# Performance work log

Measured on AMD Instinct MI355X. Metric: run time of the kernel, lower is better.

The kernel has to match this reference:

```python
import jax, jax.numpy as jnp
import numpy as np

B = 32768
IN_DIM = 768
HIDDENS = [2048, 1024, 512]
EMBED_DIM = 128
NUM_EMB = 1024
DEPTH = 3


def setup_inputs() -> dict:
    key = jax.random.key(0)
    ks = jax.random.split(key, 20)
    d = {"x": jax.random.normal(ks[0], (B, IN_DIM), dtype=jnp.float32)}
    # Encoder: in -> h0 -> h1 -> h2 -> embed  (weights stored as [in, out])
    enc_dims = [IN_DIM] + HIDDENS + [EMBED_DIM]
    for i in range(4):
        fan_in = enc_dims[i]
        d[f"enc_W{i+1}"] = jax.random.normal(ks[1 + i], (enc_dims[i], enc_dims[i + 1]), dtype=jnp.float32) / np.sqrt(fan_in)
        d[f"enc_b{i+1}"] = jnp.zeros((enc_dims[i + 1],), dtype=jnp.float32)
    # Decoder: embed -> h0 -> h1 -> h2 -> in
    dec_dims = [EMBED_DIM] + HIDDENS + [IN_DIM]
    for i in range(4):
        fan_in = dec_dims[i]
        d[f"dec_W{i+1}"] = jax.random.normal(ks[5 + i], (dec_dims[i], dec_dims[i + 1]), dtype=jnp.float32) / np.sqrt(fan_in)
        d[f"dec_b{i+1}"] = jnp.zeros((dec_dims[i + 1],), dtype=jnp.float32)
    # Codebook (nn.Embedding weight, initialized ~ N(0,1) as in the module)
    d["codebook"] = jax.random.normal(ks[9], (NUM_EMB, EMBED_DIM), dtype=jnp.float32)
    return d


def _encoder(x, W1, b1, W2, b2, W3, b3, W4, b4):
    x = jax.nn.relu(x @ W1 + b1)
    x = jax.nn.relu(x @ W2 + b2)
    x = jax.nn.relu(x @ W3 + b3)
    return x @ W4 + b4


def _decoder(x, W1, b1, W2, b2, W3, b3, W4, b4):
    x = jax.nn.relu(x @ W1 + b1)
    x = jax.nn.relu(x @ W2 + b2)
    x = jax.nn.relu(x @ W3 + b3)
    return x @ W4 + b4


def reference(x,
              enc_W1, enc_b1, enc_W2, enc_b2, enc_W3, enc_b3, enc_W4, enc_b4,
              dec_W1, dec_b1, dec_W2, dec_b2, dec_W3, dec_b3, dec_W4, dec_b4,
              codebook):
    z = _encoder(x, enc_W1, enc_b1, enc_W2, enc_b2, enc_W3, enc_b3, enc_W4, enc_b4)
    z_det = jax.lax.stop_gradient(z)

    cb_sq = jnp.sum(codebook * codebook, axis=1)  # [K]
    residue = z_det
    z_hat = jnp.zeros_like(z_det)
    codes = []
    for _ in range(DEPTH):  # residual quantization loop
        # squared L2 distances [B, K]
        dist = (jnp.sum(residue * residue, axis=1, keepdims=True)
                + cb_sq
                - 2.0 * residue @ codebook.T)
        idx = jnp.argmin(dist, axis=1)          # [B]
        codes.append(idx)
        z_hat = z_hat + codebook[idx]           # gather codebook vectors
        residue = z_det - z_hat
    all_codes = jnp.stack(codes, axis=1)        # [B, DEPTH] int

    # straight-through estimator: forward uses z_hat, grad flows through z
    z_flow = z + jax.lax.stop_gradient(z_hat - z)
    x_recon = _decoder(z_flow, dec_W1, dec_b1, dec_W2, dec_b2, dec_W3, dec_b3, dec_W4, dec_b4)
    return (x_recon, all_codes)
```

## Files before the change

kernel.cpp:

```cpp
#include <hip/hip_runtime.h>

#define FLT_MAX_C 3.402823466e+38f

typedef __attribute__((ext_vector_type(8))) __bf16 bf16x8;
typedef __attribute__((ext_vector_type(4))) float f32x4;

static __device__ __forceinline__ ushort f2bf(float x) {
    union { float f; unsigned u; } v; v.f = x;
    unsigned r = (v.u + 0x7FFFu + ((v.u >> 16) & 1u)) >> 16;
    return (ushort)r;
}

template<bool RELU, int TAG>
__global__ __launch_bounds__(256) void gemm_f32(
    const float* __restrict__ A, const float* __restrict__ W,
    const float* __restrict__ bias, float* __restrict__ C,
    int M, int K, int N)
{
    __shared__ float As[8][128];
    __shared__ float Bs[8][132];
    const int tid = threadIdx.x;
    const int bm = blockIdx.y << 7;
    const int bn = blockIdx.x << 7;

    const int la_row = tid >> 1;
    const int la_k   = (tid & 1) << 2;
    const int lb_row = tid >> 5;
    const int lb_col = (tid & 31) << 2;
    const int tm4 = (tid >> 4) << 2;
    const int tn4 = (tid & 15) << 2;

    float acc[8][8];
    #pragma unroll
    for (int i = 0; i < 8; ++i)
        #pragma unroll
        for (int j = 0; j < 8; ++j) acc[i][j] = 0.f;

    const float* aptr = A + (size_t)(bm + la_row) * K + la_k;
    const float* bptr = W + (size_t)lb_row * N + bn + lb_col;

    float4 av = *(const float4*)(aptr);
    float4 bv = *(const float4*)(bptr);

    for (int k0 = 0; k0 < K; k0 += 8) {
        __syncthreads();
        As[la_k + 0][la_row] = av.x;
        As[la_k + 1][la_row] = av.y;
        As[la_k + 2][la_row] = av.z;
        As[la_k + 3][la_row] = av.w;
        *(float4*)(&Bs[lb_row][lb_col]) = bv;
        __syncthreads();
        if (k0 + 8 < K) {
            av = *(const float4*)(aptr + k0 + 8);
            bv = *(const float4*)(bptr + (size_t)(k0 + 8) * N);
        }
        #pragma unroll
        for (int kk = 0; kk < 8; ++kk) {
            float a[8], b[8];
            *(float4*)(a)     = *(const float4*)(&As[kk][tm4]);
            *(float4*)(a + 4) = *(const float4*)(&As[kk][tm4 + 64]);
            *(float4*)(b)     = *(const float4*)(&Bs[kk][tn4]);
            *(float4*)(b + 4) = *(const float4*)(&Bs[kk][tn4 + 64]);
            #pragma unroll
            for (int i = 0; i < 8; ++i)
                #pragma unroll
                for (int j = 0; j < 8; ++j)
                    acc[i][j] = fmaf(a[i], b[j], acc[i][j]);
        }
    }

    float bv0[8];
    #pragma unroll
    for (int j = 0; j < 8; ++j)
        bv0[j] = bias[bn + tn4 + (j < 4 ? j : 60 + j)];

    #pragma unroll
    for (int i = 0; i < 8; ++i) {
        int row = bm + tm4 + (i < 4 ? i : 60 + i);
        float* cp = C + (size_t)row * N + bn + tn4;
        float4 v0, v1;
        v0.x = acc[i][0] + bv0[0]; v0.y = acc[i][1] + bv0[1];
        v0.z = acc[i][2] + bv0[2]; v0.w = acc[i][3] + bv0[3];
        v1.x = acc[i][4] + bv0[4]; v1.y = acc[i][5] + bv0[5];
        v1.z = acc[i][6] + bv0[6]; v1.w = acc[i][7] + bv0[7];
        if (RELU) {
            v0.x = fmaxf(v0.x, 0.f); v0.y = fmaxf(v0.y, 0.f);
            v0.z = fmaxf(v0.z, 0.f); v0.w = fmaxf(v0.w, 0.f);
            v1.x = fmaxf(v1.x, 0.f); v1.y = fmaxf(v1.y, 0.f);
            v1.z = fmaxf(v1.z, 0.f); v1.w = fmaxf(v1.w, 0.f);
        }
        *(float4*)(cp) = v0;
        *(float4*)(cp + 64) = v1;
    }
}

template<bool RELU, bool OUTF32, int TAG>
__global__ __launch_bounds__(256) void gemm_bf16(
    const ushort* __restrict__ A,
    const ushort* __restrict__ Wt,
    const float* __restrict__ bias,
    void* __restrict__ C,
    int M, int K, int N)
{
    __shared__ __align__(16) ushort As[128][64];
    __shared__ __align__(16) ushort Bs[128][64];
    const int tid  = threadIdx.x;
    const int lane = tid & 63;
    const int wv   = tid >> 6;
    const int wm   = (wv >> 1) << 6;
    const int wn   = (wv & 1) << 6;
    const int bm   = blockIdx.y << 7;
    const int bn   = blockIdx.x << 7;
    const int lr   = lane & 15;
    const int lh   = lane >> 4;

    f32x4 acc[4][4];
    #pragma unroll
    for (int m = 0; m < 4; ++m)
        #pragma unroll
        for (int n = 0; n < 4; ++n) acc[m][n] = (f32x4){0.f, 0.f, 0.f, 0.f};

    for (int k0 = 0; k0 < K; k0 += 64) {
        __syncthreads();
        #pragma unroll
        for (int i = 0; i < 4; ++i) {
            const int c    = wv * 4 + i;
            const int boff = c * 1024 + lane * 16;
            const int r    = boff >> 7;
            const int cbt  = boff & 127;
            const char* sa = (const char*)A  + (((size_t)(bm + r) * K + k0) << 1) + cbt;
            const char* sb = (const char*)Wt + (((size_t)(bn + r) * K + k0) << 1) + cbt;
            __builtin_amdgcn_global_load_lds((const void*)sa, (void*)(&As[0][0] + c * 512), 16, 0, 0);
            __builtin_amdgcn_global_load_lds((const void*)sb, (void*)(&Bs[0][0] + c * 512), 16, 0, 0);
        }
        __syncthreads();
        #pragma unroll
        for (int kk = 0; kk < 64; kk += 32) {
            bf16x8 af[4], bfr[4];
            #pragma unroll
            for (int m = 0; m < 4; ++m)
                af[m] = *(const bf16x8*)&As[wm + m * 16 + lr][kk + lh * 8];
            #pragma unroll
            for (int n = 0; n < 4; ++n)
                bfr[n] = *(const bf16x8*)&Bs[wn + n * 16 + lr][kk + lh * 8];
            #pragma unroll
            for (int m = 0; m < 4; ++m)
                #pragma unroll
                for (int n = 0; n < 4; ++n)
                    acc[m][n] = __builtin_amdgcn_mfma_f32_16x16x32_bf16(
                        af[m], bfr[n], acc[m][n], 0, 0, 0);
        }
    }

    #pragma unroll
    for (int n = 0; n < 4; ++n) {
        const int col = bn + wn + n * 16 + lr;
        const float bcol = bias[col];
        #pragma unroll
        for (int m = 0; m < 4; ++m) {
            #pragma unroll
            for (int i = 0; i < 4; ++i) {
                const int row = bm + wm + m * 16 + lh * 4 + i;
                float v = acc[m][n][i] + bcol;
                if (RELU) v = fmaxf(v, 0.f);
                if (OUTF32) ((float*)C)[(size_t)row * N + col] = v;
                else        ((ushort*)C)[(size_t)row * N + col] = f2bf(v);
            }
        }
    }
}

__global__ __launch_bounds__(256) void wt_convert(
    const float* __restrict__ W, ushort* __restrict__ Wt, int K, int N)
{
    __shared__ ushort t[64][65];
    const int kb = blockIdx.y << 6, nb = blockIdx.x << 6;
    const int c  = threadIdx.x & 63;
    const int r0 = (threadIdx.x >> 6) << 4;
    #pragma unroll
    for (int i = 0; i < 16; ++i)
        t[r0 + i][c] = f2bf(W[(size_t)(kb + r0 + i) * N + nb + c]);
    __syncthreads();
    #pragma unroll
    for (int i = 0; i < 16; ++i)
        Wt[(size_t)(nb + r0 + i) * K + kb + c] = t[c][r0 + i];
}

__global__ __launch_bounds__(256) void cbsq_kernel(
    const float* __restrict__ cb, float* __restrict__ cbsq)
{
    int k = blockIdx.x * 256 + threadIdx.x;
    const float* r = cb + ((size_t)k << 7);
    float s = 0.f;
    #pragma unroll 8
    for (int d = 0; d < 128; ++d) s = fmaf(r[d], r[d], s);
    cbsq[k] = s;
}

__global__ __launch_bounds__(256, 2) void quant_kernel(
    const float* __restrict__ z, const float* __restrict__ cb,
    const float* __restrict__ cbsq, ushort* __restrict__ zhat_bf,
    float* __restrict__ codes)
{
    __shared__ __align__(16) float cbl[2][4][16 * 128];
    __shared__ float sd[4][64];
    __shared__ int   si[4][64];

    const int lane = threadIdx.x & 63;
    const int wv   = threadIdx.x >> 6;
    const size_t row = (size_t)blockIdx.x * 64 + lane;
    const int kbeg = wv << 8;

    const float4* zr = (const float4*)(z + row * 128);
    float4 r[32];
    #pragma unroll
    for (int i = 0; i < 32; ++i) r[i] = zr[i];

    float mycb[4];
    #pragma unroll
    for (int j = 0; j < 4; ++j) mycb[j] = cbsq[kbeg + (j << 6) + lane];

    auto stage = [&](int c, int b) {
        const float* src = cb + ((size_t)(kbeg + (c << 4)) << 7);
        float* dst = &cbl[b][wv][0];
        #pragma unroll
        for (int i = 0; i < 8; ++i) {
            __builtin_amdgcn_global_load_lds(
                (const void*)(src + i * 256 + lane * 4),
                (void*)(dst + i * 256), 16, 0, 0);
        }
    };

    for (int t = 0; t < 3; ++t) {
        float4 rr4 = {0.f, 0.f, 0.f, 0.f};
        #pragma unroll
        for (int i = 0; i < 32; ++i) {
            rr4.x = fmaf(r[i].x, r[i].x, rr4.x);
            rr4.y = fmaf(r[i].y, r[i].y, rr4.y);
            rr4.z = fmaf(r[i].z, r[i].z, rr4.z);
            rr4.w = fmaf(r[i].w, r[i].w, rr4.w);
        }
        const float rr = (rr4.x + rr4.y) + (rr4.z + rr4.w);

        stage(0, 0);
        float bd = FLT_MAX_C; int bi = 0;
        for (int c = 0; c < 16; ++c) {
            if (c < 15) {
                stage(c + 1, (c + 1) & 1);
                asm volatile("s_waitcnt vmcnt(8)" ::: "memory");
            } else {
                asm volatile("s_waitcnt vmcnt(0)" ::: "memory");
            }
            const float* buf = cbl[c & 1][wv];
            for (int tt = 0; tt < 16; ++tt) {
                const float4* c4 = (const float4*)(buf + tt * 128);
                float4 a4 = {0.f, 0.f, 0.f, 0.f};
                #pragma unroll
                for (int i = 0; i < 32; ++i) {
                    float4 cv = c4[i];
                    a4.x = fmaf(r[i].x, cv.x, a4.x);
                    a4.y = fmaf(r[i].y, cv.y, a4.y);
                    a4.z = fmaf(r[i].z, cv.z, a4.z);
                    a4.w = fmaf(r[i].w, cv.w, a4.w);
                }
                float dot = (a4.x + a4.y) + (a4.z + a4.w);
                const int q = (c << 4) + tt;
                float cs = __shfl(mycb[q >> 6], q & 63);
                float dist = (rr + cs) - 2.f * dot;
                if (dist < bd) { bd = dist; bi = kbeg + q; }
            }
        }
        sd[wv][lane] = bd; si[wv][lane] = bi;
        __syncthreads();
        float d = sd[0][lane]; int bidx = si[0][lane];
        #pragma unroll
        for (int w = 1; w < 4; ++w) {
            float dw = sd[w][lane]; int iw = si[w][lane];
            if (dw < d) { d = dw; bidx = iw; }
        }
        __syncthreads();

        if (wv == 0) codes[row * 3 + t] = (float)bidx;

        const float4* cbest = (const float4*)(cb + ((size_t)bidx << 7));
        #pragma unroll
        for (int i = 0; i < 32; ++i) {
            float4 cv = cbest[i];
            r[i].x -= cv.x; r[i].y -= cv.y; r[i].z -= cv.z; r[i].w -= cv.w;
        }
    }

    ushort* zrow = zhat_bf + row * 128;
    #pragma unroll
    for (int i = 0; i < 8; ++i) {
        const int idx = (wv << 3) + i;
        float4 zv = zr[idx];
        ushort4 o;
        o.x = f2bf(zv.x - r[idx].x); o.y = f2bf(zv.y - r[idx].y);
        o.z = f2bf(zv.z - r[idx].z); o.w = f2bf(zv.w - r[idx].w);
        ((ushort4*)zrow)[idx] = o;
    }
}

extern "C" void kernel_launch(void* const* d_in, const int* in_sizes, int n_in,
                              void* d_out, int out_size, void* d_ws, size_t ws_size,
                              hipStream_t stream)
{
    const float* x   = (const float*)d_in[0];
    const float* eW1 = (const float*)d_in[1];
    const float* eb1 = (const float*)d_in[2];
    const float* eW2 = (const float*)d_in[3];
    const float* eb2 = (const float*)d_in[4];
    const float* eW3 = (const float*)d_in[5];
    const float* eb3 = (const float*)d_in[6];
    const float* eW4 = (const float*)d_in[7];
    const float* eb4 = (const float*)d_in[8];
    const float* dW1 = (const float*)d_in[9];
    const float* db1 = (const float*)d_in[10];
    const float* dW2 = (const float*)d_in[11];
    const float* db2 = (const float*)d_in[12];
    const float* dW3 = (const float*)d_in[13];
    const float* db3 = (const float*)d_in[14];
    const float* dW4 = (const float*)d_in[15];
    const float* db4 = (const float*)d_in[16];
    const float* cb  = (const float*)d_in[17];

    float* out   = (float*)d_out;
    float* codes = out + (size_t)32768 * 768;

    ushort* Wt1 = (ushort*)d_ws;
    ushort* Wt2 = Wt1 + (size_t)2048 * 128;
    ushort* Wt3 = Wt2 + (size_t)1024 * 2048;
    ushort* Wt4 = Wt3 + (size_t)512 * 1024;
    float*  sq  = (float*)(Wt4 + (size_t)768 * 512);
    float*  act = sq + 1024;
    const size_t fixed_b = (char*)act - (char*)d_ws;

    int mc = 32768;
    while (mc > 1024) {
        if (fixed_b + (size_t)mc * 15104 <= ws_size) break;
        mc >>= 1;
    }

    float*  R1  = act;
    float*  R2  = R1 + (size_t)mc * 2048;
    float*  R3  = R2 + (size_t)mc * 1024;
    float*  RZ  = R3 + (size_t)mc * 512;
    ushort* ZHb = (ushort*)(RZ + (size_t)mc * 128);
    ushort* D1  = (ushort*)R1;
    ushort* D2  = (ushort*)R2;
    ushort* D3  = (ushort*)R3;

    wt_convert<<<dim3(2048 / 64, 128 / 64), 256, 0, stream>>>(dW1, Wt1, 128, 2048);
    wt_convert<<<dim3(1024 / 64, 2048 / 64), 256, 0, stream>>>(dW2, Wt2, 2048, 1024);
    wt_convert<<<dim3(512 / 64, 1024 / 64), 256, 0, stream>>>(dW3, Wt3, 1024, 512);
    wt_convert<<<dim3(768 / 64, 512 / 64), 256, 0, stream>>>(dW4, Wt4, 512, 768);
    cbsq_kernel<<<4, 256, 0, stream>>>(cb, sq);

    const int mg = mc >> 7;
    for (int r0 = 0; r0 < 32768; r0 += mc) {
        const float* xi     = x     + (size_t)r0 * 768;
        float*       outi   = out   + (size_t)r0 * 768;
        float*       codesi = codes + (size_t)r0 * 3;
        gemm_f32<true , 1><<<dim3(16, mg), 256, 0, stream>>>(xi, eW1, eb1, R1, mc, 768,  2048);
        gemm_f32<true , 2><<<dim3( 8, mg), 256, 0, stream>>>(R1, eW2, eb2, R2, mc, 2048, 1024);
        gemm_f32<true , 3><<<dim3( 4, mg), 256, 0, stream>>>(R2, eW3, eb3, R3, mc, 1024, 512);
        gemm_f32<false, 4><<<dim3( 1, mg), 256, 0, stream>>>(R3, eW4, eb4, RZ, mc, 512,  128);
        quant_kernel<<<mc >> 6, 256, 0, stream>>>(RZ, cb, sq, ZHb, codesi);
        gemm_bf16<true , false, 5><<<dim3(16, mg), 256, 0, stream>>>(ZHb, Wt1, db1, D1,   mc, 128,  2048);
        gemm_bf16<true , false, 6><<<dim3( 8, mg), 256, 0, stream>>>(D1,  Wt2, db2, D2,   mc, 2048, 1024);
        gemm_bf16<true , false, 7><<<dim3( 4, mg), 256, 0, stream>>>(D2,  Wt3, db3, D3,   mc, 1024, 512);
        gemm_bf16<false, true , 8><<<dim3( 6, mg), 256, 0, stream>>>(D3,  Wt4, db4, outi, mc, 512,  768);
    }
}
```

Baseline: 4.421 ms.

## Deepen FP32 GEMM K-tile, add 64-row final encoder GEMM, split quantizer rows across lanes

The FP32 encoder GEMM now stages 16 K-elements per shared-memory round instead of 8, halving barrier count per K. The encoder's last layer (N=128) gets a 64-row tile variant so twice as many blocks launch. The quantizer now assigns two lanes per row, each handling half of the embedding dimension and combining partial dots with a shuffle, so each wave covers more codebook entries with fewer registers. GEMMs are also specialized as per-layer kernels with compile-time K and N. Risks are higher shared memory and register use per GEMM block, and extra shuffles in the quantizer's inner loop.

After: 5.422 ms. +22.7%, slower.

```diff
diff --git a/kernel.cpp b/kernel.cpp
--- a/kernel.cpp
+++ b/kernel.cpp
@@ -11,14 +11,13 @@
     return (ushort)r;
 }
 
-template<bool RELU, int TAG>
-__global__ __launch_bounds__(256) void gemm_f32(
+template<bool RELU>
+__device__ __forceinline__ void gemm_f32_dev(
     const float* __restrict__ A, const float* __restrict__ W,
-    const float* __restrict__ bias, float* __restrict__ C,
-    int M, int K, int N)
-{
-    __shared__ float As[8][128];
-    __shared__ float Bs[8][132];
+    const float* __restrict__ bias, float* __restrict__ C, int K, int N)
+{
+    __shared__ float As[16][128];
+    __shared__ float Bs[16][132];
     const int tid = threadIdx.x;
     const int bm = blockIdx.y << 7;
     const int bn = blockIdx.x << 7;
@@ -39,23 +38,32 @@
     const float* aptr = A + (size_t)(bm + la_row) * K + la_k;
     const float* bptr = W + (size_t)lb_row * N + bn + lb_col;
 
-    float4 av = *(const float4*)(aptr);
-    float4 bv = *(const float4*)(bptr);
-
-    for (int k0 = 0; k0 < K; k0 += 8) {
-        __syncthreads();
-        As[la_k + 0][la_row] = av.x;
-        As[la_k + 1][la_row] = av.y;
-        As[la_k + 2][la_row] = av.z;
-        As[la_k + 3][la_row] = av.w;
-        *(float4*)(&Bs[lb_row][lb_col]) = bv;
-        __syncthreads();
-        if (k0 + 8 < K) {
-            av = *(const float4*)(aptr + k0 + 8);
-            bv = *(const float4*)(bptr + (size_t)(k0 + 8) * N);
-        }
-        #pragma unroll
-        for (int kk = 0; kk < 8; ++kk) {
+    float4 av0 = *(const float4*)(aptr);
+    float4 av1 = *(const float4*)(aptr + 8);
+    float4 bv0 = *(const float4*)(bptr);
+    float4 bv1 = *(const float4*)(bptr + (size_t)8 * N);
+
+    for (int k0 = 0; k0 < K; k0 += 16) {
+        __syncthreads();
+        As[la_k + 0][la_row] = av0.x;
+        As[la_k + 1][la_row] = av0.y;
+        As[la_k + 2][la_row] = av0.z;
+        As[la_k + 3][la_row] = av0.w;
+        As[la_k + 8][la_row] = av1.x;
+        As[la_k + 9][la_row] = av1.y;
+        As[la_k + 10][la_row] = av1.z;
+        As[la_k + 11][la_row] = av1.w;
+        *(float4*)(&Bs[lb_row][lb_col]) = bv0;
+        *(float4*)(&Bs[lb_row + 8][lb_col]) = bv1;
+        __syncthreads();
+        if (k0 + 16 < K) {
+            av0 = *(const float4*)(aptr + k0 + 16);
+            av1 = *(const float4*)(aptr + k0 + 24);
+            bv0 = *(const float4*)(bptr + (size_t)(k0 + 16) * N);
+            bv1 = *(const float4*)(bptr + (size_t)(k0 + 24) * N);
+        }
+        #pragma unroll
+        for (int kk = 0; kk < 16; ++kk) {
             float a[8], b[8];
             *(float4*)(a)     = *(const float4*)(&As[kk][tm4]);
             *(float4*)(a + 4) = *(const float4*)(&As[kk][tm4 + 64]);
@@ -69,20 +77,20 @@
         }
     }
 
-    float bv0[8];
+    float bv[8];
     #pragma unroll
     for (int j = 0; j < 8; ++j)
-        bv0[j] = bias[bn + tn4 + (j < 4 ? j : 60 + j)];
+        bv[j] = bias[bn + tn4 + (j < 4 ? j : 60 + j)];
 
     #pragma unroll
     for (int i = 0; i < 8; ++i) {
         int row = bm + tm4 + (i < 4 ? i : 60 + i);
         float* cp = C + (size_t)row * N + bn + tn4;
         float4 v0, v1;
-        v0.x = acc[i][0] + bv0[0]; v0.y = acc[i][1] + bv0[1];
-        v0.z = acc[i][2] + bv0[2]; v0.w = acc[i][3] + bv0[3];
-        v1.x = acc[i][4] + bv0[4]; v1.y = acc[i][5] + bv0[5];
-        v1.z = acc[i][6] + bv0[6]; v1.w = acc[i][7] + bv0[7];
+        v0.x = acc[i][0] + bv[0]; v0.y = acc[i][1] + bv[1];
+        v0.z = acc[i][2] + bv[2]; v0.w = acc[i][3] + bv[3];
+        v1.x = acc[i][4] + bv[4]; v1.y = acc[i][5] + bv[5];
+        v1.z = acc[i][6] + bv[6]; v1.w = acc[i][7] + bv[7];
         if (RELU) {
             v0.x = fmaxf(v0.x, 0.f); v0.y = fmaxf(v0.y, 0.f);
             v0.z = fmaxf(v0.z, 0.f); v0.w = fmaxf(v0.w, 0.f);
@@ -94,13 +102,93 @@
     }
 }
 
-template<bool RELU, bool OUTF32, int TAG>
-__global__ __launch_bounds__(256) void gemm_bf16(
-    const ushort* __restrict__ A,
-    const ushort* __restrict__ Wt,
-    const float* __restrict__ bias,
-    void* __restrict__ C,
-    int M, int K, int N)
+template<bool RELU>
+__device__ __forceinline__ void gemm_f32_64_dev(
+    const float* __restrict__ A, const float* __restrict__ W,
+    const float* __restrict__ bias, float* __restrict__ C, int K, int N)
+{
+    __shared__ float As[16][64];
+    __shared__ float Bs[16][132];
+    const int tid = threadIdx.x;
+    const int bm = blockIdx.y << 6;
+    const int bn = blockIdx.x << 7;
+
+    const int la_row = tid & 63;
+    const int la_k   = (tid >> 6) << 2;
+    const int lb_row = tid >> 5;
+    const int lb_col = (tid & 31) << 2;
+    const int tr = tid >> 4;
+    const int tc = tid & 15;
+
+    float acc[4][8];
+    #pragma unroll
+    for (int i = 0; i < 4; ++i)
+        #pragma unroll
+        for (int j = 0; j < 8; ++j) acc[i][j] = 0.f;
+
+    const float* aptr = A + (size_t)(bm + la_row) * K + la_k;
+    const float* bptr = W + (size_t)lb_row * N + bn + lb_col;
+
+    float4 av = *(const float4*)(aptr);
+    float4 bv0 = *(const float4*)(bptr);
+    float4 bv1 = *(const float4*)(bptr + (size_t)8 * N);
+
+    for (int k0 = 0; k0 < K; k0 += 16) {
+        __syncthreads();
+        As[la_k + 0][la_row] = av.x;
+        As[la_k + 1][la_row] = av.y;
+        As[la_k + 2][la_row] = av.z;
+        As[la_k + 3][la_row] = av.w;
+        *(float4*)(&Bs[lb_row][lb_col]) = bv0;
+        *(float4*)(&Bs[lb_row + 8][lb_col]) = bv1;
+        __syncthreads();
+        if (k0 + 16 < K) {
+            av  = *(const float4*)(aptr + k0 + 16);
+            bv0 = *(const float4*)(bptr + (size_t)(k0 + 16) * N);
+            bv1 = *(const float4*)(bptr + (size_t)(k0 + 24) * N);
+        }
+        #pragma unroll
+        for (int kk = 0; kk < 16; ++kk) {
+            float a[4], b[8];
+            *(float4*)(a) = *(const float4*)(&As[kk][tr << 2]);
+            *(float4*)(b)     = *(const float4*)(&Bs[kk][tc << 2]);
+            *(float4*)(b + 4) = *(const float4*)(&Bs[kk][(tc << 2) + 64]);
+            #pragma unroll
+            for (int i = 0; i < 4; ++i)
+                #pragma unroll
+                for (int j = 0; j < 8; ++j)
+                    acc[i][j] = fmaf(a[i], b[j], acc[i][j]);
+        }
+    }
+
+    float bb[8];
+    #pragma unroll
+    for (int j = 0; j < 8; ++j)
+        bb[j] = bias[bn + (tc << 2) + (j < 4 ? j : 60 + j)];
+
+    #pragma unroll
+    for (int i = 0; i < 4; ++i) {
+        float* cp = C + (size_t)(bm + (tr << 2) + i) * N + bn + (tc << 2);
+        float4 v0, v1;
+        v0.x = acc[i][0] + bb[0]; v0.y = acc[i][1] + bb[1];
+        v0.z = acc[i][2] + bb[2]; v0.w = acc[i][3] + bb[3];
+        v1.x = acc[i][4] + bb[4]; v1.y = acc[i][5] + bb[5];
+        v1.z = acc[i][6] + bb[6]; v1.w = acc[i][7] + bb[7];
+        if (RELU) {
+            v0.x = fmaxf(v0.x, 0.f); v0.y = fmaxf(v0.y, 0.f);
+            v0.z = fmaxf(v0.z, 0.f); v0.w = fmaxf(v0.w, 0.f);
+            v1.x = fmaxf(v1.x, 0.f); v1.y = fmaxf(v1.y, 0.f);
+            v1.z = fmaxf(v1.z, 0.f); v1.w = fmaxf(v1.w, 0.f);
+        }
+        *(float4*)(cp) = v0;
+        *(float4*)(cp + 64) = v1;
+    }
+}
+
+template<bool RELU, bool OUTF32>
+__device__ __forceinline__ void gemm_bf16_dev(
+    const ushort* __restrict__ A, const ushort* __restrict__ Wt,
+    const float* __restrict__ bias, void* __restrict__ C, int K, int N)
 {
     __shared__ __align__(16) ushort As[128][64];
     __shared__ __align__(16) ushort Bs[128][64];
@@ -170,6 +258,23 @@
     }
 }
 
+__global__ __launch_bounds__(256) void enc1_gemm(const float* A, const float* W, const float* b, float* C)
+{ gemm_f32_dev<true>(A, W, b, C, 768, 2048); }
+__global__ __launch_bounds__(256) void enc2_gemm(const float* A, const float* W, const float* b, float* C)
+{ gemm_f32_dev<true>(A, W, b, C, 2048, 1024); }
+__global__ __launch_bounds__(256) void enc3_gemm(const float* A, const float* W, const float* b, float* C)
+{ gemm_f32_dev<true>(A, W, b, C, 1024, 512); }
+__global__ __launch_bounds__(256) void enc4_gemm(const float* A, const float* W, const float* b, float* C)
+{ gemm_f32_64_dev<false>(A, W, b, C, 512, 128); }
+__global__ __launch_bounds__(256) void dec1_gemm(const ushort* A, const ushort* Wt, const float* b, void* C)
+{ gemm_bf16_dev<true, false>(A, Wt, b, C, 128, 2048); }
+__global__ __launch_bounds__(256) void dec2_gemm(const ushort* A, const ushort* Wt, const float* b, void* C)
+{ gemm_bf16_dev<true, false>(A, Wt, b, C, 2048, 1024); }
+__global__ __launch_bounds__(256) void dec3_gemm(const ushort* A, const ushort* Wt, const float* b, void* C)
+{ gemm_bf16_dev<true, false>(A, Wt, b, C, 1024, 512); }
+__global__ __launch_bounds__(256) void dec4_gemm(const ushort* A, const ushort* Wt, const float* b, void* C)
+{ gemm_bf16_dev<false, true>(A, Wt, b, C, 512, 768); }
+
 __global__ __launch_bounds__(256) void wt_convert(
     const float* __restrict__ W, ushort* __restrict__ Wt, int K, int N)
 {
@@ -197,7 +302,7 @@
     cbsq[k] = s;
 }
 
-__global__ __launch_bounds__(256, 2) void quant_kernel(
+__global__ __launch_bounds__(256, 2) void rq_quant(
     const float* __restrict__ z, const float* __restrict__ cb,
     const float* __restrict__ cbsq, ushort* __restrict__ zhat_bf,
     float* __restrict__ codes)
@@ -205,20 +310,23 @@
     __shared__ __align__(16) float cbl[2][4][16 * 128];
     __shared__ float sd[4][64];
     __shared__ int   si[4][64];
+    __shared__ int   sbi[64];
 
     const int lane = threadIdx.x & 63;
     const int wv   = threadIdx.x >> 6;
-    const size_t row = (size_t)blockIdx.x * 64 + lane;
-    const int kbeg = wv << 8;
-
-    const float4* zr = (const float4*)(z + row * 128);
-    float4 r[32];
-    #pragma unroll
-    for (int i = 0; i < 32; ++i) r[i] = zr[i];
-
-    float mycb[4];
-    #pragma unroll
-    for (int j = 0; j < 4; ++j) mycb[j] = cbsq[kbeg + (j << 6) + lane];
+    const int half = lane & 1;
+    const int rib  = ((wv & 1) << 5) + (lane >> 1);
+    const size_t row = (size_t)blockIdx.x * 64 + rib;
+    const int kbeg = (wv >> 1) << 9;
+
+    const float4* zr = (const float4*)(z + row * 128) + half * 16;
+    float4 r[16];
+    #pragma unroll
+    for (int i = 0; i < 16; ++i) r[i] = zr[i];
+
+    float mycb[8];
+    #pragma unroll
+    for (int j = 0; j < 8; ++j) mycb[j] = cbsq[kbeg + (j << 6) + lane];
 
     auto stage = [&](int c, int b) {
         const float* src = cb + ((size_t)(kbeg + (c << 4)) << 7);
@@ -234,71 +342,76 @@
     for (int t = 0; t < 3; ++t) {
         float4 rr4 = {0.f, 0.f, 0.f, 0.f};
         #pragma unroll
-        for (int i = 0; i < 32; ++i) {
+        for (int i = 0; i < 16; ++i) {
             rr4.x = fmaf(r[i].x, r[i].x, rr4.x);
             rr4.y = fmaf(r[i].y, r[i].y, rr4.y);
             rr4.z = fmaf(r[i].z, r[i].z, rr4.z);
             rr4.w = fmaf(r[i].w, r[i].w, rr4.w);
         }
-        const float rr = (rr4.x + rr4.y) + (rr4.z + rr4.w);
+        float rrh = (rr4.x + rr4.y) + (rr4.z + rr4.w);
+        const float rr = rrh + __shfl_xor(rrh, 1);
 
         stage(0, 0);
         float bd = FLT_MAX_C; int bi = 0;
-        for (int c = 0; c < 16; ++c) {
-            if (c < 15) {
+        for (int c = 0; c < 32; ++c) {
+            if (c < 31) {
                 stage(c + 1, (c + 1) & 1);
                 asm volatile("s_waitcnt vmcnt(8)" ::: "memory");
             } else {
                 asm volatile("s_waitcnt vmcnt(0)" ::: "memory");
             }
-            const float* buf = cbl[c & 1][wv];
+            const float* buf = cbl[c & 1][wv] + half * 64;
+            #pragma unroll 4
             for (int tt = 0; tt < 16; ++tt) {
                 const float4* c4 = (const float4*)(buf + tt * 128);
                 float4 a4 = {0.f, 0.f, 0.f, 0.f};
                 #pragma unroll
-                for (int i = 0; i < 32; ++i) {
+                for (int i = 0; i < 16; ++i) {
                     float4 cv = c4[i];
                     a4.x = fmaf(r[i].x, cv.x, a4.x);
                     a4.y = fmaf(r[i].y, cv.y, a4.y);
                     a4.z = fmaf(r[i].z, cv.z, a4.z);
                     a4.w = fmaf(r[i].w, cv.w, a4.w);
                 }
-                float dot = (a4.x + a4.y) + (a4.z + a4.w);
+                float dh = (a4.x + a4.y) + (a4.z + a4.w);
+                float dot = dh + __shfl_xor(dh, 1);
                 const int q = (c << 4) + tt;
                 float cs = __shfl(mycb[q >> 6], q & 63);
                 float dist = (rr + cs) - 2.f * dot;
                 if (dist < bd) { bd = dist; bi = kbeg + q; }
             }
         }
-        sd[wv][lane] = bd; si[wv][lane] = bi;
-        __syncthreads();
-        float d = sd[0][lane]; int bidx = si[0][lane];
-        #pragma unroll
-        for (int w = 1; w < 4; ++w) {
-            float dw = sd[w][lane]; int iw = si[w][lane];
-            if (dw < d) { d = dw; bidx = iw; }
-        }
-        __syncthreads();
-
-        if (wv == 0) codes[row * 3 + t] = (float)bidx;
-
-        const float4* cbest = (const float4*)(cb + ((size_t)bidx << 7));
-        #pragma unroll
-        for (int i = 0; i < 32; ++i) {
+        sd[wv][rib] = bd; si[wv][rib] = bi;
+        __syncthreads();
+        if (threadIdx.x < 64) {
+            const int rr_ = threadIdx.x;
+            const int w0 = (rr_ < 32) ? 0 : 1;
+            float d = sd[w0][rr_]; int b = si[w0][rr_];
+            float d2 = sd[w0 + 2][rr_]; int b2 = si[w0 + 2][rr_];
+            if (d2 < d) { d = d2; b = b2; }
+            sbi[rr_] = b;
+            codes[((size_t)blockIdx.x * 64 + rr_) * 3 + t] = (float)b;
+        }
+        __syncthreads();
+        const int bidx = sbi[rib];
+        const float4* cbest = (const float4*)(cb + ((size_t)bidx << 7)) + half * 16;
+        #pragma unroll
+        for (int i = 0; i < 16; ++i) {
             float4 cv = cbest[i];
             r[i].x -= cv.x; r[i].y -= cv.y; r[i].z -= cv.z; r[i].w -= cv.w;
         }
     }
 
-    ushort* zrow = zhat_bf + row * 128;
-    #pragma unroll
-    for (int i = 0; i < 8; ++i) {
-        const int idx = (wv << 3) + i;
-        float4 zv = zr[idx];
-        ushort4 o;
-        o.x = f2bf(zv.x - r[idx].x); o.y = f2bf(zv.y - r[idx].y);
-        o.z = f2bf(zv.z - r[idx].z); o.w = f2bf(zv.w - r[idx].w);
-        ((ushort4*)zrow)[idx] = o;
+    if (wv < 2) {
+        ushort* zrow = zhat_bf + row * 128 + half * 64;
+        #pragma unroll
+        for (int i = 0; i < 16; ++i) {
+            float4 zv = zr[i];
+            ushort4 o;
+            o.x = f2bf(zv.x - r[i].x); o.y = f2bf(zv.y - r[i].y);
+            o.z = f2bf(zv.z - r[i].z); o.w = f2bf(zv.w - r[i].w);
+            ((ushort4*)zrow)[i] = o;
+        }
     }
 }
 
@@ -362,14 +475,14 @@
         const float* xi     = x     + (size_t)r0 * 768;
         float*       outi   = out   + (size_t)r0 * 768;
         float*       codesi = codes + (size_t)r0 * 3;
-        gemm_f32<true , 1><<<dim3(16, mg), 256, 0, stream>>>(xi, eW1, eb1, R1, mc, 768,  2048);
-        gemm_f32<true , 2><<<dim3( 8, mg), 256, 0, stream>>>(R1, eW2, eb2, R2, mc, 2048, 1024);
-        gemm_f32<true , 3><<<dim3( 4, mg), 256, 0, stream>>>(R2, eW3, eb3, R3, mc, 1024, 512);
-        gemm_f32<false, 4><<<dim3( 1, mg), 256, 0, stream>>>(R3, eW4, eb4, RZ, mc, 512,  128);
-        quant_kernel<<<mc >> 6, 256, 0, stream>>>(RZ, cb, sq, ZHb, codesi);
-        gemm_bf16<true , false, 5><<<dim3(16, mg), 256, 0, stream>>>(ZHb, Wt1, db1, D1,   mc, 128,  2048);
-        gemm_bf16<true , false, 6><<<dim3( 8, mg), 256, 0, stream>>>(D1,  Wt2, db2, D2,   mc, 2048, 1024);
-        gemm_bf16<true , false, 7><<<dim3( 4, mg), 256, 0, stream>>>(D2,  Wt3, db3, D3,   mc, 1024, 512);
-        gemm_bf16<false, true , 8><<<dim3( 6, mg), 256, 0, stream>>>(D3,  Wt4, db4, outi, mc, 512,  768);
-    }
-}
+        enc1_gemm<<<dim3(16, mg), 256, 0, stream>>>(xi, eW1, eb1, R1);
+        enc2_gemm<<<dim3( 8, mg), 256, 0, stream>>>(R1, eW2, eb2, R2);
+        enc3_gemm<<<dim3( 4, mg), 256, 0, stream>>>(R2, eW3, eb3, R3);
+        enc4_gemm<<<dim3( 1, mc >> 6), 256, 0, stream>>>(R3, eW4, eb4, RZ);
+        rq_quant<<<mc >> 6, 256, 0, stream>>>(RZ, cb, sq, ZHb, codesi);
+        dec1_gemm<<<dim3(16, mg), 256, 0, stream>>>(ZHb, Wt1, db1, D1);
+        dec2_gemm<<<dim3( 8, mg), 256, 0, stream>>>(D1,  Wt2, db2, D2);
+        dec3_gemm<<<dim3( 4, mg), 256, 0, stream>>>(D2,  Wt3, db3, D3);
+        dec4_gemm<<<dim3( 6, mg), 256, 0, stream>>>(D3,  Wt4, db4, outi);
+    }
+}
```
